# Optimization experiments

Hardware: AMD Instinct MI355X
Metric: run time of the kernel (lower is better)

Reference implementation:

```python
import jax, jax.numpy as jnp
import numpy as np

N_NODES = 50000
N_REL = 8
D_IN = 128
D_OUT = 128
N_EDGES = 800000


def setup_inputs() -> dict:
    key = jax.random.key(0)
    k = jax.random.split(key, 6)
    # Xavier-ish scales for the learned params
    w_scale = (6.0 / (D_IN + D_OUT)) ** 0.5
    X = jax.random.normal(k[0], (N_NODES, D_IN), dtype=jnp.float32)
    W = jax.random.uniform(k[1], (N_REL, D_IN, D_OUT), dtype=jnp.float32,
                           minval=-w_scale, maxval=w_scale)
    W0 = jax.random.uniform(k[2], (D_IN, D_OUT), dtype=jnp.float32,
                            minval=-w_scale, maxval=w_scale)
    inv_norm = jnp.ones((N_REL, N_NODES), dtype=jnp.float32)  # init'd to ones in torch
    # COO edge list encoding the stacked sparse adjacency tensor adj_tensor[r, dst, src]
    edge_src = jax.random.randint(k[3], (N_EDGES,), 0, N_NODES, dtype=jnp.int32)
    edge_dst = jax.random.randint(k[4], (N_EDGES,), 0, N_NODES, dtype=jnp.int32)
    edge_rel = jax.random.randint(k[5], (N_EDGES,), 0, N_REL, dtype=jnp.int32)
    return {"X": X, "W": W, "W0": W0, "inv_norm": inv_norm,
            "edge_src": edge_src, "edge_dst": edge_dst, "edge_rel": edge_rel}


def reference(X, W, W0, inv_norm, edge_src, edge_dst, edge_rel) -> jnp.ndarray:
    # Per relation r:  inv_norm[r][:,None] * (A_r @ (X @ W[r]))  ; summed over r
    R, N = inv_norm.shape
    # Dense per-relation transform: [R, N, D_OUT]
    XW = jnp.einsum('nd,rde->rne', X, W)
    # Sparse A_r @ XW_r as gather over source nodes + scatter-add into (rel, dst)
    msgs = XW[edge_rel, edge_src]                       # [E, D_OUT]
    seg_ids = edge_rel * N + edge_dst                   # combined (rel, dst) segment id
    agg = jax.ops.segment_sum(msgs, seg_ids, num_segments=R * N)
    agg = agg.reshape(R, N, -1)                         # [R, N, D_OUT]
    incoming = jnp.sum(agg * inv_norm[:, :, None], axis=0)  # [N, D_OUT]
    self_connection = X @ W0
    return incoming + self_connection
```

## Files before the change

### kernel.cpp

```cpp
#include <hip/hip_runtime.h>

typedef __attribute__((ext_vector_type(8))) short short8;
typedef __attribute__((ext_vector_type(4))) float f32x4;

__device__ __forceinline__ unsigned short f2bf(float f) {
    unsigned u = __float_as_uint(f);
    u += 0x7FFF + ((u >> 16) & 1);
    return (unsigned short)(u >> 16);
}

__device__ __forceinline__ float readlane_f(float v, int l) {
    return __int_as_float(__builtin_amdgcn_readlane(__float_as_int(v), l));
}

__device__ __forceinline__ float bflo(unsigned u) { return __uint_as_float(u << 16); }
__device__ __forceinline__ float bfhi(unsigned u) { return __uint_as_float(u & 0xFFFF0000u); }

__device__ __forceinline__ void gld_lds16(const void* g, void* l) {
    __builtin_amdgcn_global_load_lds(
        (const __attribute__((address_space(1))) unsigned*)g,
        (__attribute__((address_space(3))) unsigned*)l, 16, 0, 0);
}

#define CHB 2048
__global__ __launch_bounds__(256) void chist_kernel(
    const int* __restrict__ edst, int* __restrict__ ccounts, int E, int C)
{
    __shared__ int lh[CHB];
    const int t = threadIdx.x;
    for (int i = t; i < C; i += 256) lh[i] = 0;
    __syncthreads();
    const int base = blockIdx.x * 2048;
    const int end = min(base + 2048, E);
    for (int i = base + t; i < end; i += 256)
        atomicAdd(&lh[edst[i] >> 8], 1);
    __syncthreads();
    for (int i = t; i < C; i += 256)
        if (lh[i]) atomicAdd(&ccounts[i], lh[i]);
}

__global__ __launch_bounds__(256) void cscan_kernel(
    const int* __restrict__ ccounts, int* __restrict__ cstarts,
    int* __restrict__ cursor, int C)
{
    __shared__ int sd[256];
    const int t = threadIdx.x;
    const int per = (C + 255) >> 8;
    int c[8]; int s = 0;
#pragma unroll
    for (int k = 0; k < 8; ++k) {
        const int idx = t * per + k;
        c[k] = (k < per && idx < C) ? ccounts[idx] : 0;
        s += c[k];
    }
    sd[t] = s; __syncthreads();
    for (int off = 1; off < 256; off <<= 1) {
        int x = (t >= off) ? sd[t - off] : 0;
        __syncthreads();
        sd[t] += x;
        __syncthreads();
    }
    int run = sd[t] - s;
#pragma unroll
    for (int k = 0; k < 8; ++k) {
        const int idx = t * per + k;
        if (k < per && idx < C) { cstarts[idx] = run; cursor[idx] = run; }
        run += c[k];
    }
}

#define PART_EPB 2048
__global__ __launch_bounds__(256) void partition_kernel(
    const int* __restrict__ esrc, const int* __restrict__ edst,
    const int* __restrict__ erel, int* __restrict__ cursor,
    unsigned* __restrict__ staged, int E, int C)
{
    __shared__ int lh[CHB];
    const int t = threadIdx.x;
    const int base = blockIdx.x * PART_EPB;
    const int end = min(base + PART_EPB, E);

    for (int i = t; i < C; i += 256) lh[i] = 0;
    __syncthreads();
    for (int i = base + t; i < end; i += 256)
        atomicAdd(&lh[edst[i] >> 8], 1);
    __syncthreads();
    for (int i = t; i < C; i += 256) {
        const int c = lh[i];
        lh[i] = c ? atomicAdd(&cursor[i], c) : 0;
    }
    __syncthreads();
    for (int i = base + t; i < end; i += 256) {
        const int d = edst[i];
        const int pos = atomicAdd(&lh[d >> 8], 1);
        staged[pos] = (unsigned)esrc[i] | ((unsigned)(d & 255) << 21)
                    | ((unsigned)erel[i] << 29);
    }
}

__global__ __launch_bounds__(256) void binsortcast_kernel(
    const unsigned* __restrict__ staged, const int* __restrict__ cstarts,
    int* __restrict__ starts, unsigned* __restrict__ sorted,
    int N, int E, int C,
    const float* __restrict__ X, const float* __restrict__ W,
    const float* __restrict__ W0, unsigned short* __restrict__ Xb,
    unsigned short* __restrict__ Bt, int R)
{
    __shared__ int lcur[2048];
    __shared__ int wsum[256];
    const int t = threadIdx.x;

    if (blockIdx.x >= C) {
        const int ktot = (R + 1) * 128;
        const int nx = N * 32;
        const int idx = (blockIdx.x - C) * 256 + t;
        if (idx < nx) {
            const float4 v = ((const float4*)X)[idx];
            uint2 p;
            p.x = (unsigned)f2bf(v.x) | ((unsigned)f2bf(v.y) << 16);
            p.y = (unsigned)f2bf(v.z) | ((unsigned)f2bf(v.w) << 16);
            *(uint2*)(Xb + (size_t)idx * 4) = p;
        } else if (idx < nx + 128 * ktot) {
            const int e = idx - nx;
            const int n = e / ktot;
            const int k = e - n * ktot;
            const float v = (k < R * 128) ? W[(size_t)k * 128 + n]
                                          : W0[(size_t)(k - R * 128) * 128 + n];
            Bt[(size_t)n * ktot + k] = f2bf(v);
        }
        return;
    }

    const int b = blockIdx.x;
    const int d0 = b << 8;
    const int binBase = d0 * 8;
    const int nbins = (min(d0 + 256, N) - d0) * 8;
    const int base = cstarts[b];
    const int end = (b + 1 < C) ? cstarts[b + 1] : E;

    for (int i = t; i < 2048; i += 256) lcur[i] = 0;
    __syncthreads();
    for (int i = base + t; i < end; i += 256) {
        const unsigned v = staged[i];
        atomicAdd(&lcur[(int)((v >> 21) & 255u) * 8 + (int)(v >> 29)], 1);
    }
    __syncthreads();
    const int b8 = t * 8;
    int c[8]; int s = 0;
#pragma unroll
    for (int k = 0; k < 8; ++k) { c[k] = lcur[b8 + k]; s += c[k]; }
    wsum[t] = s; __syncthreads();
    for (int off = 1; off < 256; off <<= 1) {
        int x = (t >= off) ? wsum[t - off] : 0;
        __syncthreads();
        wsum[t] += x;
        __syncthreads();
    }
    int run = wsum[t] - s + base;
#pragma unroll
    for (int k = 0; k < 8; ++k) {
        lcur[b8 + k] = run;
        if (b8 + k < nbins) starts[binBase + b8 + k] = run;
        run += c[k];
    }
    __syncthreads();
    for (int i = base + t; i < end; i += 256) {
        const unsigned v = staged[i];
        const unsigned src = v & 0x1FFFFFu;
        const unsigned rel = v >> 29;
        const int pos = atomicAdd(&lcur[(int)((v >> 21) & 255u) * 8 + (int)rel], 1);
        sorted[pos] = src | (rel << 28);
    }
}

#define ACC(P, U) switch ((P) >> 28) {                                   \
        case 0: ax0 += bflo(U); ay0 += bfhi(U); break;                   \
        case 1: ax1 += bflo(U); ay1 += bfhi(U); break;                   \
        case 2: ax2 += bflo(U); ay2 += bfhi(U); break;                   \
        case 3: ax3 += bflo(U); ay3 += bfhi(U); break;                   \
        case 4: ax4 += bflo(U); ay4 += bfhi(U); break;                   \
        case 5: ax5 += bflo(U); ay5 += bfhi(U); break;                   \
        case 6: ax6 += bflo(U); ay6 += bfhi(U); break;                   \
        default: ax7 += bflo(U); ay7 += bfhi(U); break; }

__global__ __launch_bounds__(256) void aggregate_kernel(
    const unsigned short* __restrict__ Xb, const float* __restrict__ inv_norm,
    const unsigned* __restrict__ sorted, const int* __restrict__ starts,
    unsigned short* __restrict__ A, int N, int E)
{
    const int dst = (int)((blockIdx.x * blockDim.x + threadIdx.x) >> 6);
    if (dst >= N) return;
    const int lane = threadIdx.x & 63;

    const int start = starts[dst * 8];
    const int end = (dst + 1 < N) ? starts[dst * 8 + 8] : E;

    float ax0=0,ay0=0, ax1=0,ay1=0, ax2=0,ay2=0, ax3=0,ay3=0;
    float ax4=0,ay4=0, ax5=0,ay5=0, ax6=0,ay6=0, ax7=0,ay7=0;

    for (int cb = start; cb < end; cb += 64) {
        const int take = min(64, end - cb);
        unsigned batch = 0;
        if (cb + lane < end) batch = sorted[cb + lane];
        int j = 0;
        for (; j + 16 <= take; j += 16) {
            unsigned p[16], u[16];
#pragma unroll
            for (int q = 0; q < 16; ++q)
                p[q] = (unsigned)__builtin_amdgcn_readlane((int)batch, j + q);
#pragma unroll
            for (int q = 0; q < 16; ++q)
                u[q] = ((const unsigned*)(Xb + ((size_t)(p[q] & 0x0FFFFFFFu) << 7)))[lane];
#pragma unroll
            for (int q = 0; q < 16; ++q) { ACC(p[q], u[q]); }
        }
        for (; j + 8 <= take; j += 8) {
            unsigned p[8], u[8];
#pragma unroll
            for (int q = 0; q < 8; ++q)
                p[q] = (unsigned)__builtin_amdgcn_readlane((int)batch, j + q);
#pragma unroll
            for (int q = 0; q < 8; ++q)
                u[q] = ((const unsigned*)(Xb + ((size_t)(p[q] & 0x0FFFFFFFu) << 7)))[lane];
#pragma unroll
            for (int q = 0; q < 8; ++q) { ACC(p[q], u[q]); }
        }
        for (; j + 4 <= take; j += 4) {
            const unsigned p0 = (unsigned)__builtin_amdgcn_readlane((int)batch, j);
            const unsigned p1 = (unsigned)__builtin_amdgcn_readlane((int)batch, j + 1);
            const unsigned p2 = (unsigned)__builtin_amdgcn_readlane((int)batch, j + 2);
            const unsigned p3 = (unsigned)__builtin_amdgcn_readlane((int)batch, j + 3);
            const unsigned u0 = ((const unsigned*)(Xb + ((size_t)(p0 & 0x0FFFFFFFu) << 7)))[lane];
            const unsigned u1 = ((const unsigned*)(Xb + ((size_t)(p1 & 0x0FFFFFFFu) << 7)))[lane];
            const unsigned u2 = ((const unsigned*)(Xb + ((size_t)(p2 & 0x0FFFFFFFu) << 7)))[lane];
            const unsigned u3 = ((const unsigned*)(Xb + ((size_t)(p3 & 0x0FFFFFFFu) << 7)))[lane];
            ACC(p0, u0); ACC(p1, u1); ACC(p2, u2); ACC(p3, u3);
        }
        for (; j < take; ++j) {
            const unsigned p = (unsigned)__builtin_amdgcn_readlane((int)batch, j);
            const unsigned u = ((const unsigned*)(Xb + ((size_t)(p & 0x0FFFFFFFu) << 7)))[lane];
            ACC(p, u);
        }
    }

    const float nv_l = (lane < 8) ? inv_norm[(size_t)lane * N + dst] : 0.f;

    unsigned short* Arow = A + (size_t)dst * 1024 + lane * 2;
    {
        float s;
        s = readlane_f(nv_l, 0); *(unsigned*)(Arow + 0*128) = (unsigned)f2bf(ax0*s) | ((unsigned)f2bf(ay0*s) << 16);
        s = readlane_f(nv_l, 1); *(unsigned*)(Arow + 1*128) = (unsigned)f2bf(ax1*s) | ((unsigned)f2bf(ay1*s) << 16);
        s = readlane_f(nv_l, 2); *(unsigned*)(Arow + 2*128) = (unsigned)f2bf(ax2*s) | ((unsigned)f2bf(ay2*s) << 16);
        s = readlane_f(nv_l, 3); *(unsigned*)(Arow + 3*128) = (unsigned)f2bf(ax3*s) | ((unsigned)f2bf(ay3*s) << 16);
        s = readlane_f(nv_l, 4); *(unsigned*)(Arow + 4*128) = (unsigned)f2bf(ax4*s) | ((unsigned)f2bf(ay4*s) << 16);
        s = readlane_f(nv_l, 5); *(unsigned*)(Arow + 5*128) = (unsigned)f2bf(ax5*s) | ((unsigned)f2bf(ay5*s) << 16);
        s = readlane_f(nv_l, 6); *(unsigned*)(Arow + 6*128) = (unsigned)f2bf(ax6*s) | ((unsigned)f2bf(ay6*s) << 16);
        s = readlane_f(nv_l, 7); *(unsigned*)(Arow + 7*128) = (unsigned)f2bf(ax7*s) | ((unsigned)f2bf(ay7*s) << 16);
    }
}

template <int KT>
__global__ __launch_bounds__(512) void gemm_kernel(
    const unsigned short* __restrict__ A, const unsigned short* __restrict__ Xb,
    const unsigned short* __restrict__ Bt, float* __restrict__ out, int M)
{
    constexpr int NI = KT / 64;
    constexpr int NA = (KT - 128) / 64;
    __shared__ unsigned short Asw[2][128 * 64];
    __shared__ unsigned short Bsw[2][128 * 64];

    const int tid = threadIdx.x;
    const int wave = tid >> 6;
    const int lane = tid & 63;
    const int ln = lane & 15, quad = lane >> 4;
    const int wm = wave & 3;
    const int wn = wave >> 2;
    const int m0 = blockIdx.x * 128;

    const int lr = lane >> 3;
    const int lc = lane & 7;
    const int r0 = wave * 16 + lr;
    const int r1 = wave * 16 + 8 + lr;
    int am0 = m0 + r0; if (am0 >= M) am0 = M - 1;
    int am1 = m0 + r1; if (am1 >= M) am1 = M - 1;
    const unsigned short* pA0 = A  + (size_t)am0 * (KT - 128) + ((lc ^ (r0 & 7)) << 3);
    const unsigned short* pA1 = A  + (size_t)am1 * (KT - 128) + ((lc ^ (r1 & 7)) << 3);
    const unsigned short* pX0 = Xb + (size_t)am0 * 128        + ((lc ^ (r0 & 7)) << 3);
    const unsigned short* pX1 = Xb + (size_t)am1 * 128        + ((lc ^ (r1 & 7)) << 3);
    const unsigned short* pB0 = Bt + (size_t)r0 * KT          + ((lc ^ (r0 & 7)) << 3);
    const unsigned short* pB1 = Bt + (size_t)r1 * KT          + ((lc ^ (r1 & 7)) << 3);

    f32x4 acc[8] = {};

    auto issue = [&](int ko, int buf) {
        const unsigned short* a0 = (ko < NA) ? (pA0 + ko * 64) : (pX0 + (ko - NA) * 64);
        const unsigned short* a1 = (ko < NA) ? (pA1 + ko * 64) : (pX1 + (ko - NA) * 64);
        gld_lds16(a0,           &Asw[buf][(wave * 16 + 0) * 64]);
        gld_lds16(a1,           &Asw[buf][(wave * 16 + 8) * 64]);
        gld_lds16(pB0 + ko * 64, &Bsw[buf][(wave * 16 + 0) * 64]);
        gld_lds16(pB1 + ko * 64, &Bsw[buf][(wave * 16 + 8) * 64]);
    };
    auto mfma_phase = [&](int buf) {
#pragma unroll
        for (int ks = 0; ks < 2; ++ks) {
            short8 af[2], bf[4];
#pragma unroll
            for (int mi = 0; mi < 2; ++mi) {
                const int r = wm * 32 + mi * 16 + ln;
                af[mi] = *(const short8*)&Asw[buf][r * 64 + ((((ks << 2) + quad) ^ (r & 7)) << 3)];
            }
#pragma unroll
            for (int ci = 0; ci < 4; ++ci) {
                const int r = wn * 64 + ci * 16 + ln;
                bf[ci] = *(const short8*)&Bsw[buf][r * 64 + ((((ks << 2) + quad) ^ (r & 7)) << 3)];
            }
#pragma unroll
            for (int mi = 0; mi < 2; ++mi)
#pragma unroll
                for (int ci = 0; ci < 4; ++ci)
                    acc[mi * 4 + ci] = __builtin_amdgcn_mfma_f32_16x16x32_bf16(
                        af[mi], bf[ci], acc[mi * 4 + ci], 0, 0, 0);
        }
    };

    issue(0, 0);
    __syncthreads();

    int cur = 0;
#pragma unroll
    for (int ko = 0; ko < NI; ++ko) {
        if (ko + 1 < NI) issue(ko + 1, cur ^ 1);
        __builtin_amdgcn_sched_barrier(0);
        mfma_phase(cur);
        __syncthreads();
        cur ^= 1;
    }

#pragma unroll
    for (int mi = 0; mi < 2; ++mi)
#pragma unroll
        for (int ci = 0; ci < 4; ++ci)
#pragma unroll
            for (int rg = 0; rg < 4; ++rg) {
                const int row = m0 + wm * 32 + mi * 16 + quad * 4 + rg;
                if (row < M)
                    out[(size_t)row * 128 + wn * 64 + ci * 16 + ln] = acc[mi * 4 + ci][rg];
            }
}

__global__ __launch_bounds__(256) void gemm_kernel_rt(
    const unsigned short* __restrict__ A, const unsigned short* __restrict__ Xb,
    const unsigned short* __restrict__ Bt, float* __restrict__ out,
    int M, int ktot)
{
    const int tid = threadIdx.x;
    const int wave = tid >> 6;
    const int lane = tid & 63;
    const int ln = lane & 15, quad = lane >> 4;
    const int m0 = blockIdx.x * 64 + wave * 16;
    int m = m0 + ln; if (m >= M) m = M - 1;
    const unsigned short* Arow = A + (size_t)m * (ktot - 128) + quad * 8;
    const unsigned short* Xrow = Xb + (size_t)m * 128 + quad * 8;
    const unsigned short* Bbase = Bt + (size_t)ln * ktot + quad * 8;

    f32x4 acc[8] = {};
    for (int kb = 0; kb < (ktot >> 5); ++kb) {
        const int k0 = kb << 5;
        const unsigned short* asrc = (k0 < ktot - 128) ? (Arow + k0) : (Xrow + (k0 - (ktot - 128)));
        const short8 a = *(const short8*)asrc;
#pragma unroll
        for (int c = 0; c < 8; ++c) {
            const short8 b = *(const short8*)(Bbase + (size_t)c * 16 * ktot + k0);
            acc[c] = __builtin_amdgcn_mfma_f32_16x16x32_bf16(a, b, acc[c], 0, 0, 0);
        }
    }
#pragma unroll
    for (int c = 0; c < 8; ++c) {
#pragma unroll
        for (int rg = 0; rg < 4; ++rg) {
            const int row = m0 + quad * 4 + rg;
            if (row < M) out[(size_t)row * 128 + c * 16 + ln] = acc[c][rg];
        }
    }
}

extern "C" void kernel_launch(void* const* d_in, const int* in_sizes, int n_in,
                              void* d_out, int out_size, void* d_ws, size_t ws_size,
                              hipStream_t stream) {
    const float* X        = (const float*)d_in[0];
    const float* W        = (const float*)d_in[1];
    const float* W0       = (const float*)d_in[2];
    const float* inv_norm = (const float*)d_in[3];
    const int*   esrc     = (const int*)d_in[4];
    const int*   edst     = (const int*)d_in[5];
    const int*   erel     = (const int*)d_in[6];
    float* out = (float*)d_out;

    const int N  = in_sizes[0] / 128;
    const int E  = in_sizes[4];
    const int R  = in_sizes[3] / N;
    const int KB = N * 8;
    const int ktot = (R + 1) * 128;
    const int C  = (N + 255) >> 8;

    char* ws = (char*)d_ws;
    size_t off = 0;
    auto alloc = [&](size_t bytes) -> char* {
        char* p = ws + off; off = (off + bytes + 255) & ~(size_t)255; return p;
    };
    unsigned short* A         = (unsigned short*)alloc((size_t)N * R * 128 * 2);
    unsigned short* Xb        = (unsigned short*)alloc((size_t)N * 128 * 2);
    unsigned short* Bt        = (unsigned short*)alloc((size_t)128 * ktot * 2);
    int*            ccounts   = (int*)alloc((size_t)C * 4);
    int*            cstarts   = (int*)alloc((size_t)C * 4);
    int*            cursor    = (int*)alloc((size_t)C * 4);
    int*            starts    = (int*)alloc((size_t)KB * 4);
    unsigned*       staged    = (unsigned*)alloc((size_t)E * 4);
    unsigned*       sorted    = (unsigned*)alloc((size_t)E * 4);
    (void)ws_size;

    const int nEdgeBlocks = (E + 2047) / 2048;
    const int nCastBlocks = (N * 32 + 128 * ktot + 255) / 256;

    hipMemsetAsync(ccounts, 0, (size_t)C * 4, stream);
    chist_kernel<<<nEdgeBlocks, 256, 0, stream>>>(edst, ccounts, E, C);
    cscan_kernel<<<1, 256, 0, stream>>>(ccounts, cstarts, cursor, C);
    partition_kernel<<<nEdgeBlocks, 256, 0, stream>>>(esrc, edst, erel, cursor, staged, E, C);
    binsortcast_kernel<<<C + nCastBlocks, 256, 0, stream>>>(
        staged, cstarts, starts, sorted, N, E, C, X, W, W0, Xb, Bt, R);
    aggregate_kernel<<<(N + 3) / 4, 256, 0, stream>>>(Xb, inv_norm, sorted, starts, A, N, E);
    if (ktot == 1152)
        gemm_kernel<1152><<<(N + 127) / 128, 512, 0, stream>>>(A, Xb, Bt, out, N);
    else
        gemm_kernel_rt<<<(N + 63) / 64, 256, 0, stream>>>(A, Xb, Bt, out, N, ktot);
}
```

Measured before the change: 195.0 us.

## Overlap second-half aggregation with first-half GEMM in a combined kernel

Splits the destination nodes into two halves. The first half is aggregated alone, then one combined launch runs the GEMM for the first half in some blocks while the other blocks aggregate the second half, and a final GEMM covers the second half. The aim is to overlap the memory-bound gather with the MFMA-bound GEMM and so fill idle compute units. The cost is an extra launch and a larger mixed kernel whose 512-thread blocks and LDS allocation now also apply to the aggregation waves, which may lower occupancy for that work. The 4-wide unrolled tail of the aggregation loop is also dropped.

```diff
diff --git a/kernel.cpp b/kernel.cpp
--- a/kernel.cpp
+++ b/kernel.cpp
@@ -183,86 +183,75 @@
         case 6: ax6 += bflo(U); ay6 += bfhi(U); break;                   \
         default: ax7 += bflo(U); ay7 += bfhi(U); break; }
 
+#define AGG_WAVE_BODY(DST)                                                        \
+    const int start = starts[(DST) * 8];                                          \
+    const int end = ((DST) + 1 < N) ? starts[(DST) * 8 + 8] : E;                  \
+    float ax0=0,ay0=0, ax1=0,ay1=0, ax2=0,ay2=0, ax3=0,ay3=0;                     \
+    float ax4=0,ay4=0, ax5=0,ay5=0, ax6=0,ay6=0, ax7=0,ay7=0;                     \
+    for (int cb = start; cb < end; cb += 64) {                                    \
+        const int take = min(64, end - cb);                                       \
+        unsigned batch = 0;                                                       \
+        if (cb + lane < end) batch = sorted[cb + lane];                           \
+        int j = 0;                                                                \
+        for (; j + 16 <= take; j += 16) {                                         \
+            unsigned p[16], u[16];                                                \
+            _Pragma("unroll")                                                     \
+            for (int q = 0; q < 16; ++q)                                          \
+                p[q] = (unsigned)__builtin_amdgcn_readlane((int)batch, j + q);    \
+            _Pragma("unroll")                                                     \
+            for (int q = 0; q < 16; ++q)                                          \
+                u[q] = ((const unsigned*)(Xb + ((size_t)(p[q] & 0x0FFFFFFFu) << 7)))[lane]; \
+            _Pragma("unroll")                                                     \
+            for (int q = 0; q < 16; ++q) { ACC(p[q], u[q]); }                     \
+        }                                                                         \
+        for (; j + 8 <= take; j += 8) {                                           \
+            unsigned p[8], u[8];                                                  \
+            _Pragma("unroll")                                                     \
+            for (int q = 0; q < 8; ++q)                                           \
+                p[q] = (unsigned)__builtin_amdgcn_readlane((int)batch, j + q);    \
+            _Pragma("unroll")                                                     \
+            for (int q = 0; q < 8; ++q)                                           \
+                u[q] = ((const unsigned*)(Xb + ((size_t)(p[q] & 0x0FFFFFFFu) << 7)))[lane]; \
+            _Pragma("unroll")                                                     \
+            for (int q = 0; q < 8; ++q) { ACC(p[q], u[q]); }                      \
+        }                                                                         \
+        for (; j < take; ++j) {                                                   \
+            const unsigned p = (unsigned)__builtin_amdgcn_readlane((int)batch, j);\
+            const unsigned u = ((const unsigned*)(Xb + ((size_t)(p & 0x0FFFFFFFu) << 7)))[lane]; \
+            ACC(p, u);                                                            \
+        }                                                                         \
+    }                                                                             \
+    const float nv_l = (lane < 8) ? inv_norm[(size_t)lane * N + (DST)] : 0.f;     \
+    unsigned short* Arow = A + (size_t)(DST) * 1024 + lane * 2;                   \
+    {                                                                             \
+        float s;                                                                  \
+        s = readlane_f(nv_l, 0); *(unsigned*)(Arow + 0*128) = (unsigned)f2bf(ax0*s) | ((unsigned)f2bf(ay0*s) << 16); \
+        s = readlane_f(nv_l, 1); *(unsigned*)(Arow + 1*128) = (unsigned)f2bf(ax1*s) | ((unsigned)f2bf(ay1*s) << 16); \
+        s = readlane_f(nv_l, 2); *(unsigned*)(Arow + 2*128) = (unsigned)f2bf(ax2*s) | ((unsigned)f2bf(ay2*s) << 16); \
+        s = readlane_f(nv_l, 3); *(unsigned*)(Arow + 3*128) = (unsigned)f2bf(ax3*s) | ((unsigned)f2bf(ay3*s) << 16); \
+        s = readlane_f(nv_l, 4); *(unsigned*)(Arow + 4*128) = (unsigned)f2bf(ax4*s) | ((unsigned)f2bf(ay4*s) << 16); \
+        s = readlane_f(nv_l, 5); *(unsigned*)(Arow + 5*128) = (unsigned)f2bf(ax5*s) | ((unsigned)f2bf(ay5*s) << 16); \
+        s = readlane_f(nv_l, 6); *(unsigned*)(Arow + 6*128) = (unsigned)f2bf(ax6*s) | ((unsigned)f2bf(ay6*s) << 16); \
+        s = readlane_f(nv_l, 7); *(unsigned*)(Arow + 7*128) = (unsigned)f2bf(ax7*s) | ((unsigned)f2bf(ay7*s) << 16); \
+    }
+
 __global__ __launch_bounds__(256) void aggregate_kernel(
     const unsigned short* __restrict__ Xb, const float* __restrict__ inv_norm,
     const unsigned* __restrict__ sorted, const int* __restrict__ starts,
-    unsigned short* __restrict__ A, int N, int E)
+    unsigned short* __restrict__ A, int N, int E, int dstEnd)
 {
     const int dst = (int)((blockIdx.x * blockDim.x + threadIdx.x) >> 6);
-    if (dst >= N) return;
+    if (dst >= dstEnd) return;
     const int lane = threadIdx.x & 63;
-
-    const int start = starts[dst * 8];
-    const int end = (dst + 1 < N) ? starts[dst * 8 + 8] : E;
-
-    float ax0=0,ay0=0, ax1=0,ay1=0, ax2=0,ay2=0, ax3=0,ay3=0;
-    float ax4=0,ay4=0, ax5=0,ay5=0, ax6=0,ay6=0, ax7=0,ay7=0;
-
-    for (int cb = start; cb < end; cb += 64) {
-        const int take = min(64, end - cb);
-        unsigned batch = 0;
-        if (cb + lane < end) batch = sorted[cb + lane];
-        int j = 0;
-        for (; j + 16 <= take; j += 16) {
-            unsigned p[16], u[16];
-#pragma unroll
-            for (int q = 0; q < 16; ++q)
-                p[q] = (unsigned)__builtin_amdgcn_readlane((int)batch, j + q);
-#pragma unroll
-            for (int q = 0; q < 16; ++q)
-                u[q] = ((const unsigned*)(Xb + ((size_t)(p[q] & 0x0FFFFFFFu) << 7)))[lane];
-#pragma unroll
-            for (int q = 0; q < 16; ++q) { ACC(p[q], u[q]); }
-        }
-        for (; j + 8 <= take; j += 8) {
-            unsigned p[8], u[8];
-#pragma unroll
-            for (int q = 0; q < 8; ++q)
-                p[q] = (unsigned)__builtin_amdgcn_readlane((int)batch, j + q);
-#pragma unroll
-            for (int q = 0; q < 8; ++q)
-                u[q] = ((const unsigned*)(Xb + ((size_t)(p[q] & 0x0FFFFFFFu) << 7)))[lane];
-#pragma unroll
-            for (int q = 0; q < 8; ++q) { ACC(p[q], u[q]); }
-        }
-        for (; j + 4 <= take; j += 4) {
-            const unsigned p0 = (unsigned)__builtin_amdgcn_readlane((int)batch, j);
-            const unsigned p1 = (unsigned)__builtin_amdgcn_readlane((int)batch, j + 1);
-            const unsigned p2 = (unsigned)__builtin_amdgcn_readlane((int)batch, j + 2);
-            const unsigned p3 = (unsigned)__builtin_amdgcn_readlane((int)batch, j + 3);
-            const unsigned u0 = ((const unsigned*)(Xb + ((size_t)(p0 & 0x0FFFFFFFu) << 7)))[lane];
-            const unsigned u1 = ((const unsigned*)(Xb + ((size_t)(p1 & 0x0FFFFFFFu) << 7)))[lane];
-            const unsigned u2 = ((const unsigned*)(Xb + ((size_t)(p2 & 0x0FFFFFFFu) << 7)))[lane];
-            const unsigned u3 = ((const unsigned*)(Xb + ((size_t)(p3 & 0x0FFFFFFFu) << 7)))[lane];
-            ACC(p0, u0); ACC(p1, u1); ACC(p2, u2); ACC(p3, u3);
-        }
-        for (; j < take; ++j) {
-            const unsigned p = (unsigned)__builtin_amdgcn_readlane((int)batch, j);
-            const unsigned u = ((const unsigned*)(Xb + ((size_t)(p & 0x0FFFFFFFu) << 7)))[lane];
-            ACC(p, u);
-        }
-    }
-
-    const float nv_l = (lane < 8) ? inv_norm[(size_t)lane * N + dst] : 0.f;
-
-    unsigned short* Arow = A + (size_t)dst * 1024 + lane * 2;
-    {
-        float s;
-        s = readlane_f(nv_l, 0); *(unsigned*)(Arow + 0*128) = (unsigned)f2bf(ax0*s) | ((unsigned)f2bf(ay0*s) << 16);
-        s = readlane_f(nv_l, 1); *(unsigned*)(Arow + 1*128) = (unsigned)f2bf(ax1*s) | ((unsigned)f2bf(ay1*s) << 16);
-        s = readlane_f(nv_l, 2); *(unsigned*)(Arow + 2*128) = (unsigned)f2bf(ax2*s) | ((unsigned)f2bf(ay2*s) << 16);
-        s = readlane_f(nv_l, 3); *(unsigned*)(Arow + 3*128) = (unsigned)f2bf(ax3*s) | ((unsigned)f2bf(ay3*s) << 16);
-        s = readlane_f(nv_l, 4); *(unsigned*)(Arow + 4*128) = (unsigned)f2bf(ax4*s) | ((unsigned)f2bf(ay4*s) << 16);
-        s = readlane_f(nv_l, 5); *(unsigned*)(Arow + 5*128) = (unsigned)f2bf(ax5*s) | ((unsigned)f2bf(ay5*s) << 16);
-        s = readlane_f(nv_l, 6); *(unsigned*)(Arow + 6*128) = (unsigned)f2bf(ax6*s) | ((unsigned)f2bf(ay6*s) << 16);
-        s = readlane_f(nv_l, 7); *(unsigned*)(Arow + 7*128) = (unsigned)f2bf(ax7*s) | ((unsigned)f2bf(ay7*s) << 16);
-    }
+    AGG_WAVE_BODY(dst)
 }
 
 template <int KT>
-__global__ __launch_bounds__(512) void gemm_kernel(
-    const unsigned short* __restrict__ A, const unsigned short* __restrict__ Xb,
-    const unsigned short* __restrict__ Bt, float* __restrict__ out, int M)
+__global__ __launch_bounds__(512) void aggemm_kernel(
+    const unsigned short* __restrict__ Xb, const float* __restrict__ inv_norm,
+    const unsigned* __restrict__ sorted, const int* __restrict__ starts,
+    unsigned short* __restrict__ A, const unsigned short* __restrict__ Bt,
+    float* __restrict__ out, int N, int E, int H1, int nG)
 {
     constexpr int NI = KT / 64;
     constexpr int NA = (KT - 128) / 64;
@@ -272,10 +261,19 @@
     const int tid = threadIdx.x;
     const int wave = tid >> 6;
     const int lane = tid & 63;
+
+    if ((int)blockIdx.x >= nG) {
+        const int dst = H1 + ((int)blockIdx.x - nG) * 8 + wave;
+        if (dst >= N) return;
+        AGG_WAVE_BODY(dst)
+        return;
+    }
+
     const int ln = lane & 15, quad = lane >> 4;
     const int wm = wave & 3;
     const int wn = wave >> 2;
     const int m0 = blockIdx.x * 128;
+    const int M = N;
 
     const int lr = lane >> 3;
     const int lc = lane & 7;
@@ -295,8 +293,98 @@
     auto issue = [&](int ko, int buf) {
         const unsigned short* a0 = (ko < NA) ? (pA0 + ko * 64) : (pX0 + (ko - NA) * 64);
         const unsigned short* a1 = (ko < NA) ? (pA1 + ko * 64) : (pX1 + (ko - NA) * 64);
-        gld_lds16(a0,           &Asw[buf][(wave * 16 + 0) * 64]);
-        gld_lds16(a1,           &Asw[buf][(wave * 16 + 8) * 64]);
+        gld_lds16(a0,            &Asw[buf][(wave * 16 + 0) * 64]);
+        gld_lds16(a1,            &Asw[buf][(wave * 16 + 8) * 64]);
+        gld_lds16(pB0 + ko * 64, &Bsw[buf][(wave * 16 + 0) * 64]);
+        gld_lds16(pB1 + ko * 64, &Bsw[buf][(wave * 16 + 8) * 64]);
+    };
+    auto mfma_phase = [&](int buf) {
+#pragma unroll
+        for (int ks = 0; ks < 2; ++ks) {
+            short8 af[2], bf[4];
+#pragma unroll
+            for (int mi = 0; mi < 2; ++mi) {
+                const int r = wm * 32 + mi * 16 + ln;
+                af[mi] = *(const short8*)&Asw[buf][r * 64 + ((((ks << 2) + quad) ^ (r & 7)) << 3)];
+            }
+#pragma unroll
+            for (int ci = 0; ci < 4; ++ci) {
+                const int r = wn * 64 + ci * 16 + ln;
+                bf[ci] = *(const short8*)&Bsw[buf][r * 64 + ((((ks << 2) + quad) ^ (r & 7)) << 3)];
+            }
+#pragma unroll
+            for (int mi = 0; mi < 2; ++mi)
+#pragma unroll
+                for (int ci = 0; ci < 4; ++ci)
+                    acc[mi * 4 + ci] = __builtin_amdgcn_mfma_f32_16x16x32_bf16(
+                        af[mi], bf[ci], acc[mi * 4 + ci], 0, 0, 0);
+        }
+    };
+
+    issue(0, 0);
+    __syncthreads();
+
+    int cur = 0;
+#pragma unroll
+    for (int ko = 0; ko < NI; ++ko) {
+        if (ko + 1 < NI) issue(ko + 1, cur ^ 1);
+        __builtin_amdgcn_sched_barrier(0);
+        mfma_phase(cur);
+        __syncthreads();
+        cur ^= 1;
+    }
+
+#pragma unroll
+    for (int mi = 0; mi < 2; ++mi)
+#pragma unroll
+        for (int ci = 0; ci < 4; ++ci)
+#pragma unroll
+            for (int rg = 0; rg < 4; ++rg) {
+                const int row = m0 + wm * 32 + mi * 16 + quad * 4 + rg;
+                if (row < M)
+                    out[(size_t)row * 128 + wn * 64 + ci * 16 + ln] = acc[mi * 4 + ci][rg];
+            }
+}
+
+template <int KT>
+__global__ __launch_bounds__(512) void gemm_kernel(
+    const unsigned short* __restrict__ A, const unsigned short* __restrict__ Xb,
+    const unsigned short* __restrict__ Bt, float* __restrict__ out,
+    int M, int mBase)
+{
+    constexpr int NI = KT / 64;
+    constexpr int NA = (KT - 128) / 64;
+    __shared__ unsigned short Asw[2][128 * 64];
+    __shared__ unsigned short Bsw[2][128 * 64];
+
+    const int tid = threadIdx.x;
+    const int wave = tid >> 6;
+    const int lane = tid & 63;
+    const int ln = lane & 15, quad = lane >> 4;
+    const int wm = wave & 3;
+    const int wn = wave >> 2;
+    const int m0 = mBase + blockIdx.x * 128;
+
+    const int lr = lane >> 3;
+    const int lc = lane & 7;
+    const int r0 = wave * 16 + lr;
+    const int r1 = wave * 16 + 8 + lr;
+    int am0 = m0 + r0; if (am0 >= M) am0 = M - 1;
+    int am1 = m0 + r1; if (am1 >= M) am1 = M - 1;
+    const unsigned short* pA0 = A  + (size_t)am0 * (KT - 128) + ((lc ^ (r0 & 7)) << 3);
+    const unsigned short* pA1 = A  + (size_t)am1 * (KT - 128) + ((lc ^ (r1 & 7)) << 3);
+    const unsigned short* pX0 = Xb + (size_t)am0 * 128        + ((lc ^ (r0 & 7)) << 3);
+    const unsigned short* pX1 = Xb + (size_t)am1 * 128        + ((lc ^ (r1 & 7)) << 3);
+    const unsigned short* pB0 = Bt + (size_t)r0 * KT          + ((lc ^ (r0 & 7)) << 3);
+    const unsigned short* pB1 = Bt + (size_t)r1 * KT          + ((lc ^ (r1 & 7)) << 3);
+
+    f32x4 acc[8] = {};
+
+    auto issue = [&](int ko, int buf) {
+        const unsigned short* a0 = (ko < NA) ? (pA0 + ko * 64) : (pX0 + (ko - NA) * 64);
+        const unsigned short* a1 = (ko < NA) ? (pA1 + ko * 64) : (pX1 + (ko - NA) * 64);
+        gld_lds16(a0,            &Asw[buf][(wave * 16 + 0) * 64]);
+        gld_lds16(a1,            &Asw[buf][(wave * 16 + 8) * 64]);
         gld_lds16(pB0 + ko * 64, &Bsw[buf][(wave * 16 + 0) * 64]);
         gld_lds16(pB1 + ko * 64, &Bsw[buf][(wave * 16 + 8) * 64]);
     };
@@ -428,9 +516,23 @@
     partition_kernel<<<nEdgeBlocks, 256, 0, stream>>>(esrc, edst, erel, cursor, staged, E, C);
     binsortcast_kernel<<<C + nCastBlocks, 256, 0, stream>>>(
         staged, cstarts, starts, sorted, N, E, C, X, W, W0, Xb, Bt, R);
-    aggregate_kernel<<<(N + 3) / 4, 256, 0, stream>>>(Xb, inv_norm, sorted, starts, A, N, E);
-    if (ktot == 1152)
-        gemm_kernel<1152><<<(N + 127) / 128, 512, 0, stream>>>(A, Xb, Bt, out, N);
-    else
+
+    if (ktot == 1152 && N > 128) {
+        int nG = ((N / 2) + 127) / 128;
+        int H1 = nG * 128;
+        if (H1 > N) { H1 = N; nG = (H1 + 127) / 128; }
+        const int H2 = N - H1;
+        const int nA2 = (H2 + 7) / 8;
+        aggregate_kernel<<<(H1 + 3) / 4, 256, 0, stream>>>(
+            Xb, inv_norm, sorted, starts, A, N, E, H1);
+        aggemm_kernel<1152><<<nG + nA2, 512, 0, stream>>>(
+            Xb, inv_norm, sorted, starts, A, Bt, out, N, E, H1, nG);
+        if (H2 > 0)
+            gemm_kernel<1152><<<(H2 + 127) / 128, 512, 0, stream>>>(
+                A, Xb, Bt, out, N, H1);
+    } else {
+        aggregate_kernel<<<(N + 3) / 4, 256, 0, stream>>>(
+            Xb, inv_norm, sorted, starts, A, N, E, N);
         gemm_kernel_rt<<<(N + 63) / 64, 256, 0, stream>>>(A, Xb, Bt, out, N, ktot);
-}
+    }
+}
```

New measurement: 229.8 us. +17.9%, slower.

## Fuse histogram, scan and partition into one cooperative kernel with grid syncs

Applied to the files above, without the earlier changes.

Replaces the memset plus three small front-end launches (bin histogram, single-block scan, partition) with one cooperative kernel that uses grid-wide syncs between phases. The block-local histogram is computed once and reused for partitioning, so edst is not re-read and re-counted. The goal is to cut launch gaps and redundant work. The cost is three grid.sync barriers, and cooperative launch requires all ~391 blocks to be co-resident, with the old launch path kept as a fallback on error.

```diff
diff --git a/kernel.cpp b/kernel.cpp
--- a/kernel.cpp
+++ b/kernel.cpp
@@ -1,4 +1,7 @@
 #include <hip/hip_runtime.h>
+#include <hip/hip_cooperative_groups.h>
+
+namespace cg = cooperative_groups;
 
 typedef __attribute__((ext_vector_type(8))) short short8;
 typedef __attribute__((ext_vector_type(4))) float f32x4;
@@ -23,68 +26,59 @@
 }
 
 #define CHB 2048
-__global__ __launch_bounds__(256) void chist_kernel(
-    const int* __restrict__ edst, int* __restrict__ ccounts, int E, int C)
-{
+#define PART_EPB 2048
+__global__ __launch_bounds__(256) void front_kernel(
+    const int* __restrict__ esrc, const int* __restrict__ edst,
+    const int* __restrict__ erel, int* __restrict__ ccounts,
+    int* __restrict__ cstarts, int* __restrict__ cursor,
+    unsigned* __restrict__ staged, int E, int C)
+{
+    cg::grid_group grid = cg::this_grid();
     __shared__ int lh[CHB];
-    const int t = threadIdx.x;
-    for (int i = t; i < C; i += 256) lh[i] = 0;
-    __syncthreads();
-    const int base = blockIdx.x * 2048;
-    const int end = min(base + 2048, E);
-    for (int i = base + t; i < end; i += 256)
-        atomicAdd(&lh[edst[i] >> 8], 1);
-    __syncthreads();
-    for (int i = t; i < C; i += 256)
-        if (lh[i]) atomicAdd(&ccounts[i], lh[i]);
-}
-
-__global__ __launch_bounds__(256) void cscan_kernel(
-    const int* __restrict__ ccounts, int* __restrict__ cstarts,
-    int* __restrict__ cursor, int C)
-{
     __shared__ int sd[256];
-    const int t = threadIdx.x;
-    const int per = (C + 255) >> 8;
-    int c[8]; int s = 0;
-#pragma unroll
-    for (int k = 0; k < 8; ++k) {
-        const int idx = t * per + k;
-        c[k] = (k < per && idx < C) ? ccounts[idx] : 0;
-        s += c[k];
-    }
-    sd[t] = s; __syncthreads();
-    for (int off = 1; off < 256; off <<= 1) {
-        int x = (t >= off) ? sd[t - off] : 0;
-        __syncthreads();
-        sd[t] += x;
-        __syncthreads();
-    }
-    int run = sd[t] - s;
-#pragma unroll
-    for (int k = 0; k < 8; ++k) {
-        const int idx = t * per + k;
-        if (k < per && idx < C) { cstarts[idx] = run; cursor[idx] = run; }
-        run += c[k];
-    }
-}
-
-#define PART_EPB 2048
-__global__ __launch_bounds__(256) void partition_kernel(
-    const int* __restrict__ esrc, const int* __restrict__ edst,
-    const int* __restrict__ erel, int* __restrict__ cursor,
-    unsigned* __restrict__ staged, int E, int C)
-{
-    __shared__ int lh[CHB];
     const int t = threadIdx.x;
     const int base = blockIdx.x * PART_EPB;
     const int end = min(base + PART_EPB, E);
 
+    for (int i = blockIdx.x * 256 + t; i < C; i += gridDim.x * 256)
+        ccounts[i] = 0;
     for (int i = t; i < C; i += 256) lh[i] = 0;
     __syncthreads();
+    grid.sync();
+
     for (int i = base + t; i < end; i += 256)
         atomicAdd(&lh[edst[i] >> 8], 1);
     __syncthreads();
+    for (int i = t; i < C; i += 256)
+        if (lh[i]) atomicAdd(&ccounts[i], lh[i]);
+    grid.sync();
+
+    if (blockIdx.x == 0) {
+        const int per = (C + 255) >> 8;
+        int c[8]; int s = 0;
+#pragma unroll
+        for (int k = 0; k < 8; ++k) {
+            const int idx = t * per + k;
+            c[k] = (k < per && idx < C) ? ccounts[idx] : 0;
+            s += c[k];
+        }
+        sd[t] = s; __syncthreads();
+        for (int off = 1; off < 256; off <<= 1) {
+            int x = (t >= off) ? sd[t - off] : 0;
+            __syncthreads();
+            sd[t] += x;
+            __syncthreads();
+        }
+        int run = sd[t] - s;
+#pragma unroll
+        for (int k = 0; k < 8; ++k) {
+            const int idx = t * per + k;
+            if (k < per && idx < C) { cstarts[idx] = run; cursor[idx] = run; }
+            run += c[k];
+        }
+    }
+    grid.sync();
+
     for (int i = t; i < C; i += 256) {
         const int c = lh[i];
         lh[i] = c ? atomicAdd(&cursor[i], c) : 0;
@@ -295,8 +289,8 @@
     auto issue = [&](int ko, int buf) {
         const unsigned short* a0 = (ko < NA) ? (pA0 + ko * 64) : (pX0 + (ko - NA) * 64);
         const unsigned short* a1 = (ko < NA) ? (pA1 + ko * 64) : (pX1 + (ko - NA) * 64);
-        gld_lds16(a0,           &Asw[buf][(wave * 16 + 0) * 64]);
-        gld_lds16(a1,           &Asw[buf][(wave * 16 + 8) * 64]);
+        gld_lds16(a0,            &Asw[buf][(wave * 16 + 0) * 64]);
+        gld_lds16(a1,            &Asw[buf][(wave * 16 + 8) * 64]);
         gld_lds16(pB0 + ko * 64, &Bsw[buf][(wave * 16 + 0) * 64]);
         gld_lds16(pB1 + ko * 64, &Bsw[buf][(wave * 16 + 8) * 64]);
     };
@@ -381,6 +375,80 @@
             const int row = m0 + quad * 4 + rg;
             if (row < M) out[(size_t)row * 128 + c * 16 + ln] = acc[c][rg];
         }
+    }
+}
+
+__global__ __launch_bounds__(256) void chist_kernel(
+    const int* __restrict__ edst, int* __restrict__ ccounts, int E, int C)
+{
+    __shared__ int lh[CHB];
+    const int t = threadIdx.x;
+    for (int i = t; i < C; i += 256) lh[i] = 0;
+    __syncthreads();
+    const int base = blockIdx.x * 2048;
+    const int end = min(base + 2048, E);
+    for (int i = base + t; i < end; i += 256)
+        atomicAdd(&lh[edst[i] >> 8], 1);
+    __syncthreads();
+    for (int i = t; i < C; i += 256)
+        if (lh[i]) atomicAdd(&ccounts[i], lh[i]);
+}
+
+__global__ __launch_bounds__(256) void cscan_kernel(
+    const int* __restrict__ ccounts, int* __restrict__ cstarts,
+    int* __restrict__ cursor, int C)
+{
+    __shared__ int sd[256];
+    const int t = threadIdx.x;
+    const int per = (C + 255) >> 8;
+    int c[8]; int s = 0;
+#pragma unroll
+    for (int k = 0; k < 8; ++k) {
+        const int idx = t * per + k;
+        c[k] = (k < per && idx < C) ? ccounts[idx] : 0;
+        s += c[k];
+    }
+    sd[t] = s; __syncthreads();
+    for (int off = 1; off < 256; off <<= 1) {
+        int x = (t >= off) ? sd[t - off] : 0;
+        __syncthreads();
+        sd[t] += x;
+        __syncthreads();
+    }
+    int run = sd[t] - s;
+#pragma unroll
+    for (int k = 0; k < 8; ++k) {
+        const int idx = t * per + k;
+        if (k < per && idx < C) { cstarts[idx] = run; cursor[idx] = run; }
+        run += c[k];
+    }
+}
+
+__global__ __launch_bounds__(256) void partition_kernel(
+    const int* __restrict__ esrc, const int* __restrict__ edst,
+    const int* __restrict__ erel, int* __restrict__ cursor,
+    unsigned* __restrict__ staged, int E, int C)
+{
+    __shared__ int lh[CHB];
+    const int t = threadIdx.x;
+    const int base = blockIdx.x * PART_EPB;
+    const int end = min(base + PART_EPB, E);
+
+    for (int i = t; i < C; i += 256) lh[i] = 0;
+    __syncthreads();
+    for (int i = base + t; i < end; i += 256)
+        atomicAdd(&lh[edst[i] >> 8], 1);
+    __syncthreads();
+    for (int i = t; i < C; i += 256) {
+        const int c = lh[i];
+        lh[i] = c ? atomicAdd(&cursor[i], c) : 0;
+    }
+    __syncthreads();
+    for (int i = base + t; i < end; i += 256) {
+        const int d = edst[i];
+        const int pos = atomicAdd(&lh[d >> 8], 1);
+        staged[pos] = (unsigned)esrc[i] | ((unsigned)(d & 255) << 21)
+                    | ((unsigned)erel[i] << 29);
     }
 }
 
@@ -419,13 +487,23 @@
     unsigned*       sorted    = (unsigned*)alloc((size_t)E * 4);
     (void)ws_size;
 
-    const int nEdgeBlocks = (E + 2047) / 2048;
+    const int nEdgeBlocks = (E + PART_EPB - 1) / PART_EPB;
     const int nCastBlocks = (N * 32 + 128 * ktot + 255) / 256;
 
-    hipMemsetAsync(ccounts, 0, (size_t)C * 4, stream);
-    chist_kernel<<<nEdgeBlocks, 256, 0, stream>>>(edst, ccounts, E, C);
-    cscan_kernel<<<1, 256, 0, stream>>>(ccounts, cstarts, cursor, C);
-    partition_kernel<<<nEdgeBlocks, 256, 0, stream>>>(esrc, edst, erel, cursor, staged, E, C);
+    {
+        void* args[] = { (void*)&esrc, (void*)&edst, (void*)&erel,
+                         (void*)&ccounts, (void*)&cstarts, (void*)&cursor,
+                         (void*)&staged, (void*)&E, (void*)&C };
+        hipError_t err = hipLaunchCooperativeKernel(
+            (const void*)front_kernel, dim3(nEdgeBlocks), dim3(256),
+            args, 0, stream);
+        if (err != hipSuccess) {
+            hipMemsetAsync(ccounts, 0, (size_t)C * 4, stream);
+            chist_kernel<<<nEdgeBlocks, 256, 0, stream>>>(edst, ccounts, E, C);
+            cscan_kernel<<<1, 256, 0, stream>>>(ccounts, cstarts, cursor, C);
+            partition_kernel<<<nEdgeBlocks, 256, 0, stream>>>(esrc, edst, erel, cursor, staged, E, C);
+        }
+    }
     binsortcast_kernel<<<C + nCastBlocks, 256, 0, stream>>>(
         staged, cstarts, starts, sorted, N, E, C, X, W, W0, Xb, Bt, R);
     aggregate_kernel<<<(N + 3) / 4, 256, 0, stream>>>(Xb, inv_norm, sorted, starts, A, N, E);
```

Result: slower. 317.4 us (+62.8%).
